# Optimization experiments

Measured on AMD Instinct MI355X. Metric: run time of the kernel, lower is better.

Reference implementation:

```python
import jax, jax.numpy as jnp
import numpy as np
import math

N, L, D, H = 8192, 64, 256, 4
DH = D // H
TAU = 300.0

def setup_inputs() -> dict:
    key = jax.random.key(0)
    ks = jax.random.split(key, 16)
    tokens = jax.random.normal(ks[0], (N, L, D), dtype=jnp.float32)
    # sorted random timestamps in seconds within each patch window
    ts = jnp.sort(jax.random.uniform(ks[1], (N, L, 1), dtype=jnp.float32) * 3600.0, axis=1)
    mask = (jax.random.uniform(ks[2], (N, L, 1), dtype=jnp.float32) < 0.9).astype(jnp.float32)
    mask = mask.at[:, 0, :].set(1.0)  # guarantee at least one valid key per row
    s = 0.02
    Wq = jax.random.normal(ks[3], (D, D), dtype=jnp.float32) * s
    bq = jnp.zeros((D,), dtype=jnp.float32)
    Wk = jax.random.normal(ks[4], (D, D), dtype=jnp.float32) * s
    bk = jnp.zeros((D,), dtype=jnp.float32)
    Wv = jax.random.normal(ks[5], (D, D), dtype=jnp.float32) * s
    bv = jnp.zeros((D,), dtype=jnp.float32)
    Wo = jax.random.normal(ks[6], (D, D), dtype=jnp.float32) * s
    bo = jnp.zeros((D,), dtype=jnp.float32)
    readout = jax.random.normal(ks[7], (D,), dtype=jnp.float32)
    return {"tokens": tokens, "ts": ts, "mask": mask,
            "Wq": Wq, "bq": bq, "Wk": Wk, "bk": bk, "Wv": Wv, "bv": bv,
            "Wo": Wo, "bo": bo, "readout": readout}

def reference(tokens, ts, mask, Wq, bq, Wk, bk, Wv, bv, Wo, bo, readout):
    n, l, d = tokens.shape
    scale = 1.0 / math.sqrt(DH)
    # time-decay bias: dt = |t_i - t_j|, bias = log(exp(-dt/tau) + 1e-12)
    t = ts[..., 0]                                   # (N, L)
    dt = jnp.abs(t[:, :, None] - t[:, None, :])      # (N, L, L)
    bias = jnp.log(jnp.exp(-dt / max(TAU, 1e-6)) + 1e-12)
    def proj(x, W, b):
        return (x @ W.T + b).reshape(n, l, H, DH).transpose(0, 2, 1, 3)  # (N,H,L,DH)
    q = proj(tokens, Wq, bq)
    k = proj(tokens, Wk, bk)
    v = proj(tokens, Wv, bv)
    attn = jnp.einsum('nhqd,nhkd->nhqk', q, k) * scale + bias[:, None, :, :]
    key_pad = mask[..., 0] <= 0                      # (N, L) True = pad
    attn = jnp.where(key_pad[:, None, None, :], -1e9, attn)
    A = jax.nn.softmax(attn, axis=-1)
    out = jnp.einsum('nhqk,nhkd->nhqd', A, v).transpose(0, 2, 1, 3).reshape(n, l, d)
    out = (out @ Wo.T + bo) * mask                   # (N, L, D)
    # learned-query pooling attention over timesteps
    qh = jnp.broadcast_to(readout.reshape(1, 1, d), (n, 1, d)).reshape(n, 1, H, DH).transpose(0, 2, 1, 3)
    kh = out.reshape(n, l, H, DH).transpose(0, 2, 1, 3)  # kh == vh
    pool = jnp.einsum('nhqd,nhkd->nhqk', qh, kh) * scale  # (N,H,1,L)
    pool = jnp.where(key_pad[:, None, None, :], -1e9, pool)
    P = jax.nn.softmax(pool, axis=-1)
    pooled = jnp.einsum('nhqk,nhkd->nhqd', P, kh).transpose(0, 2, 1, 3).reshape(n, d)
    return pooled
```

## Files before the change

kernel.cpp:

```cpp
#include <hip/hip_runtime.h>
#include <hip/hip_bf16.h>


typedef __attribute__((ext_vector_type(8))) short short8;
typedef __attribute__((ext_vector_type(4))) float f32x4;

__device__ __forceinline__ unsigned short f2b(float x) {
  unsigned int u = __float_as_uint(x);
  u += 0x7FFFu + ((u >> 16) & 1u);
  return (unsigned short)(u >> 16);
}
__device__ __forceinline__ float b2f(unsigned short b) {
  return __uint_as_float(((unsigned int)b) << 16);
}

__global__ void wconv_kernel(const float* __restrict__ Wq, const float* __restrict__ Wk,
                             const float* __restrict__ Wv, const float* __restrict__ Wo,
                             unsigned short* __restrict__ dst) {
  int e = blockIdx.x * 256 + threadIdx.x;
  int row = e >> 8, col = e & 255;
  float v;
  if (row < 256)      v = Wq[(row << 8) | col];
  else if (row < 512) v = Wk[((row - 256) << 8) | col];
  else if (row < 768) v = Wv[((row - 512) << 8) | col];
  else                v = Wo[((row - 768) << 8) | col];
  dst[e] = f2b(v);
}

__global__ __launch_bounds__(256, 2) void patch_attn_kernel(
    const float* __restrict__ tokens, const float* __restrict__ ts,
    const float* __restrict__ maskp,
    const unsigned short* __restrict__ Wqkv,
    const unsigned short* __restrict__ Wob,
    const float* __restrict__ bq, const float* __restrict__ bk,
    const float* __restrict__ bv, const float* __restrict__ bo,
    const float* __restrict__ readout, float* __restrict__ outp) {
  __shared__ unsigned short Xb[64][264];
  __shared__ unsigned short Qh[64][72];
  __shared__ unsigned short Kh[64][72];
  __shared__ unsigned short VhT[64][72];
  __shared__ unsigned short Ah[64][72];
  __shared__ float tl[64];
  __shared__ float ml[64];
  __shared__ float ps[4][64];

  const int n   = blockIdx.x;
  const int tid = threadIdx.x;
  const int w   = tid >> 6;
  const int l   = tid & 63;
  const int l16 = l & 15;
  const int lq  = l >> 4;

  if (tid < 64) { tl[tid] = ts[n * 64 + tid]; ml[tid] = maskp[n * 64 + tid]; }

  const float4* Xg = (const float4*)(tokens + (size_t)n * (64 * 256));
  #pragma unroll
  for (int it = 0; it < 16; ++it) {
    int p = tid + it * 256;
    float4 v = Xg[p];
    int row = p >> 6, col = (p & 63) << 2;
    ushort4 b;
    b.x = f2b(v.x); b.y = f2b(v.y); b.z = f2b(v.z); b.w = f2b(v.w);
    *(ushort4*)&Xb[row][col] = b;
  }
  __syncthreads();

  const f32x4 fz = {0.f, 0.f, 0.f, 0.f};
  f32x4 oacc[4][4];
  #pragma unroll
  for (int a = 0; a < 4; ++a)
    #pragma unroll
    for (int bb = 0; bb < 4; ++bb) oacc[a][bb] = fz;

  #pragma unroll 1
  for (int h = 0; h < 4; ++h) {
    f32x4 qacc[4][3];
    #pragma unroll
    for (int rf = 0; rf < 4; ++rf)
      #pragma unroll
      for (int c = 0; c < 3; ++c) qacc[rf][c] = fz;

    const unsigned short* wp0 = Wqkv + (size_t)((0 * 256 + h * 64 + 16 * w + l16) * 256 + lq * 8);
    const unsigned short* wp1 = Wqkv + (size_t)((1 * 256 + h * 64 + 16 * w + l16) * 256 + lq * 8);
    const unsigned short* wp2 = Wqkv + (size_t)((2 * 256 + h * 64 + 16 * w + l16) * 256 + lq * 8);

    #pragma unroll
    for (int ks = 0; ks < 8; ++ks) {
      int k0 = ks * 32;
      short8 afr[4];
      #pragma unroll
      for (int rf = 0; rf < 4; ++rf)
        afr[rf] = *(const short8*)&Xb[16 * rf + l16][k0 + lq * 8];
      short8 bfr[3];
      bfr[0] = *(const short8*)(wp0 + k0);
      bfr[1] = *(const short8*)(wp1 + k0);
      bfr[2] = *(const short8*)(wp2 + k0);
      #pragma unroll
      for (int rf = 0; rf < 4; ++rf) {
        qacc[rf][0] = __builtin_amdgcn_mfma_f32_16x16x32_bf16(afr[rf], bfr[0], qacc[rf][0], 0, 0, 0);
        qacc[rf][1] = __builtin_amdgcn_mfma_f32_16x16x32_bf16(afr[rf], bfr[1], qacc[rf][1], 0, 0, 0);
        qacc[rf][2] = __builtin_amdgcn_mfma_f32_16x16x32_bf16(afr[rf], bfr[2], qacc[rf][2], 0, 0, 0);
      }
    }
    {
      int ncol = 16 * w + l16;
      float bqv = bq[h * 64 + ncol], bkv = bk[h * 64 + ncol], bvv = bv[h * 64 + ncol];
      #pragma unroll
      for (int rf = 0; rf < 4; ++rf) {
        #pragma unroll
        for (int i = 0; i < 4; ++i) {
          int m = 16 * rf + lq * 4 + i;
          Qh[m][ncol]  = f2b(qacc[rf][0][i] + bqv);
          Kh[m][ncol]  = f2b(qacc[rf][1][i] + bkv);
          VhT[ncol][m] = f2b(qacc[rf][2][i] + bvv);
        }
      }
    }
    __syncthreads();

    f32x4 sacc[4];
    #pragma unroll
    for (int j = 0; j < 4; ++j) sacc[j] = fz;
    #pragma unroll
    for (int ks = 0; ks < 2; ++ks) {
      int k0 = ks * 32;
      short8 aq = *(const short8*)&Qh[16 * w + l16][k0 + lq * 8];
      #pragma unroll
      for (int j = 0; j < 4; ++j) {
        short8 bk8 = *(const short8*)&Kh[16 * j + l16][k0 + lq * 8];
        sacc[j] = __builtin_amdgcn_mfma_f32_16x16x32_bf16(aq, bk8, sacc[j], 0, 0, 0);
      }
    }
    {
      float tn[4], mn[4];
      #pragma unroll
      for (int j = 0; j < 4; ++j) { tn[j] = tl[16 * j + l16]; mn[j] = ml[16 * j + l16]; }
      #pragma unroll
      for (int i = 0; i < 4; ++i) {
        int m = 16 * w + lq * 4 + i;
        float tm = tl[m];
        float sv[4];
        #pragma unroll
        for (int j = 0; j < 4; ++j) {
          float s = sacc[j][i] * 0.125f - fabsf(tm - tn[j]) * (1.0f / 300.0f);
          sv[j] = (mn[j] <= 0.0f) ? -1e9f : s;
        }
        float mx = fmaxf(fmaxf(sv[0], sv[1]), fmaxf(sv[2], sv[3]));
        #pragma unroll
        for (int x = 1; x < 16; x <<= 1) mx = fmaxf(mx, __shfl_xor(mx, x));
        float pj[4], sum = 0.f;
        #pragma unroll
        for (int j = 0; j < 4; ++j) { pj[j] = __expf(sv[j] - mx); sum += pj[j]; }
        #pragma unroll
        for (int x = 1; x < 16; x <<= 1) sum += __shfl_xor(sum, x);
        float inv = 1.0f / sum;
        #pragma unroll
        for (int j = 0; j < 4; ++j) Ah[m][16 * j + l16] = f2b(pj[j] * inv);
      }
    }
    __syncthreads();

    f32x4 pacc[4];
    #pragma unroll
    for (int j = 0; j < 4; ++j) pacc[j] = fz;
    #pragma unroll
    for (int ks = 0; ks < 2; ++ks) {
      int k0 = ks * 32;
      short8 ap = *(const short8*)&Ah[16 * w + l16][k0 + lq * 8];
      #pragma unroll
      for (int j = 0; j < 4; ++j) {
        short8 bv8 = *(const short8*)&VhT[16 * j + l16][k0 + lq * 8];
        pacc[j] = __builtin_amdgcn_mfma_f32_16x16x32_bf16(ap, bv8, pacc[j], 0, 0, 0);
      }
    }
    #pragma unroll
    for (int j = 0; j < 4; ++j)
      #pragma unroll
      for (int i = 0; i < 4; ++i)
        Qh[16 * w + lq * 4 + i][16 * j + l16] = f2b(pacc[j][i]);
    __syncthreads();

    {
      const unsigned short* wop[4];
      #pragma unroll
      for (int j = 0; j < 4; ++j)
        wop[j] = Wob + (size_t)((64 * w + 16 * j + l16) * 256 + h * 64 + lq * 8);
      #pragma unroll
      for (int ks = 0; ks < 2; ++ks) {
        int k0 = ks * 32;
        short8 ao[4];
        #pragma unroll
        for (int rf = 0; rf < 4; ++rf)
          ao[rf] = *(const short8*)&Qh[16 * rf + l16][k0 + lq * 8];
        short8 bw[4];
        #pragma unroll
        for (int j = 0; j < 4; ++j) bw[j] = *(const short8*)(wop[j] + k0);
        #pragma unroll
        for (int rf = 0; rf < 4; ++rf)
          #pragma unroll
          for (int j = 0; j < 4; ++j)
            oacc[rf][j] = __builtin_amdgcn_mfma_f32_16x16x32_bf16(ao[rf], bw[j], oacc[rf][j], 0, 0, 0);
      }
    }
    __syncthreads();
  }

  #pragma unroll
  for (int rf = 0; rf < 4; ++rf) {
    #pragma unroll
    for (int j = 0; j < 4; ++j) {
      int ncol = 64 * w + 16 * j + l16;
      float bov = bo[ncol];
      #pragma unroll
      for (int i = 0; i < 4; ++i) {
        int m = 16 * rf + lq * 4 + i;
        Xb[m][ncol] = f2b((oacc[rf][j][i] + bov) * ml[m]);
      }
    }
  }
  __syncthreads();

  {
    float acc = 0.f;
    #pragma unroll
    for (int d0 = 0; d0 < 64; d0 += 4) {
      ushort4 o4 = *(const ushort4*)&Xb[l][w * 64 + d0];
      acc += b2f(o4.x) * readout[w * 64 + d0]
           + b2f(o4.y) * readout[w * 64 + d0 + 1]
           + b2f(o4.z) * readout[w * 64 + d0 + 2]
           + b2f(o4.w) * readout[w * 64 + d0 + 3];
    }
    float logit = acc * 0.125f;
    if (ml[l] <= 0.0f) logit = -1e9f;
    float mx = logit;
    #pragma unroll
    for (int x = 1; x < 64; x <<= 1) mx = fmaxf(mx, __shfl_xor(mx, x));
    float p = __expf(logit - mx);
    float sm = p;
    #pragma unroll
    for (int x = 1; x < 64; x <<= 1) sm += __shfl_xor(sm, x);
    ps[w][l] = p / sm;
  }
  __syncthreads();
  {
    float o = 0.f;
    #pragma unroll
    for (int k = 0; k < 64; ++k) o += ps[w][k] * b2f(Xb[k][w * 64 + l]);
    outp[(size_t)n * 256 + w * 64 + l] = o;
  }
}

extern "C" void kernel_launch(void* const* d_in, const int* in_sizes, int n_in,
                              void* d_out, int out_size, void* d_ws, size_t ws_size,
                              hipStream_t stream) {
  const float* tokens  = (const float*)d_in[0];
  const float* ts      = (const float*)d_in[1];
  const float* mask    = (const float*)d_in[2];
  const float* Wq      = (const float*)d_in[3];
  const float* bq      = (const float*)d_in[4];
  const float* Wk      = (const float*)d_in[5];
  const float* bk      = (const float*)d_in[6];
  const float* Wv      = (const float*)d_in[7];
  const float* bv      = (const float*)d_in[8];
  const float* Wo      = (const float*)d_in[9];
  const float* bo      = (const float*)d_in[10];
  const float* readout = (const float*)d_in[11];
  (void)n_in; (void)out_size; (void)ws_size;

  unsigned short* Wqkv_b = (unsigned short*)d_ws;
  unsigned short* Wo_b   = Wqkv_b + 768 * 256;

  const int n_patches = in_sizes[0] / (64 * 256);

  wconv_kernel<<<1024, 256, 0, stream>>>(Wq, Wk, Wv, Wo, Wqkv_b);
  patch_attn_kernel<<<n_patches, 256, 0, stream>>>(
      tokens, ts, mask, Wqkv_b, Wo_b, bq, bk, bv, bo, readout, (float*)d_out);
}
```

Before: 1.293 ms.

## Stream tokens from global into MFMA fragments and shrink LDS for higher occupancy

```diff
diff --git a/kernel.cpp b/kernel.cpp
--- a/kernel.cpp
+++ b/kernel.cpp
@@ -12,6 +12,14 @@
 }
 __device__ __forceinline__ float b2f(unsigned short b) {
   return __uint_as_float(((unsigned int)b) << 16);
+}
+__device__ __forceinline__ short8 pack8(float4 a, float4 b) {
+  short8 r;
+  r[0] = (short)f2b(a.x); r[1] = (short)f2b(a.y);
+  r[2] = (short)f2b(a.z); r[3] = (short)f2b(a.w);
+  r[4] = (short)f2b(b.x); r[5] = (short)f2b(b.y);
+  r[6] = (short)f2b(b.z); r[7] = (short)f2b(b.w);
+  return r;
 }
 
 __global__ void wconv_kernel(const float* __restrict__ Wq, const float* __restrict__ Wk,
@@ -27,7 +35,7 @@
   dst[e] = f2b(v);
 }
 
-__global__ __launch_bounds__(256, 2) void patch_attn_kernel(
+__global__ __launch_bounds__(256, 3) void patch_attn_kernel(
     const float* __restrict__ tokens, const float* __restrict__ ts,
     const float* __restrict__ maskp,
     const unsigned short* __restrict__ Wqkv,
@@ -35,13 +43,8 @@
     const float* __restrict__ bq, const float* __restrict__ bk,
     const float* __restrict__ bv, const float* __restrict__ bo,
     const float* __restrict__ readout, float* __restrict__ outp) {
-  __shared__ unsigned short Xb[64][264];
-  __shared__ unsigned short Qh[64][72];
-  __shared__ unsigned short Kh[64][72];
-  __shared__ unsigned short VhT[64][72];
-  __shared__ unsigned short Ah[64][72];
-  __shared__ float tl[64];
-  __shared__ float ml[64];
+  __shared__ unsigned short T[4][64][72];
+  __shared__ float tl[64], ml[64], mneg[64];
   __shared__ float ps[4][64];
 
   const int n   = blockIdx.x;
@@ -51,133 +54,144 @@
   const int l16 = l & 15;
   const int lq  = l >> 4;
 
-  if (tid < 64) { tl[tid] = ts[n * 64 + tid]; ml[tid] = maskp[n * 64 + tid]; }
-
-  const float4* Xg = (const float4*)(tokens + (size_t)n * (64 * 256));
-  #pragma unroll
-  for (int it = 0; it < 16; ++it) {
-    int p = tid + it * 256;
-    float4 v = Xg[p];
-    int row = p >> 6, col = (p & 63) << 2;
-    ushort4 b;
-    b.x = f2b(v.x); b.y = f2b(v.y); b.z = f2b(v.z); b.w = f2b(v.w);
-    *(ushort4*)&Xb[row][col] = b;
+  if (tid < 64) {
+    tl[tid] = ts[n * 64 + tid];
+    float mk = maskp[n * 64 + tid];
+    ml[tid]   = mk;
+    mneg[tid] = (mk > 0.0f) ? 0.0f : -1e9f;
   }
   __syncthreads();
+
+  const float4* Xg4 = (const float4*)(tokens + (size_t)n * (64 * 256));
+  const float tq = tl[16 * w + l16];
 
   const f32x4 fz = {0.f, 0.f, 0.f, 0.f};
   f32x4 oacc[4][4];
   #pragma unroll
   for (int a = 0; a < 4; ++a)
     #pragma unroll
-    for (int bb = 0; bb < 4; ++bb) oacc[a][bb] = fz;
+    for (int b = 0; b < 4; ++b) oacc[a][b] = fz;
 
   #pragma unroll 1
   for (int h = 0; h < 4; ++h) {
-    f32x4 qacc[4][3];
-    #pragma unroll
-    for (int rf = 0; rf < 4; ++rf)
-      #pragma unroll
-      for (int c = 0; c < 3; ++c) qacc[rf][c] = fz;
-
-    const unsigned short* wp0 = Wqkv + (size_t)((0 * 256 + h * 64 + 16 * w + l16) * 256 + lq * 8);
-    const unsigned short* wp1 = Wqkv + (size_t)((1 * 256 + h * 64 + 16 * w + l16) * 256 + lq * 8);
-    const unsigned short* wp2 = Wqkv + (size_t)((2 * 256 + h * 64 + 16 * w + l16) * 256 + lq * 8);
+    f32x4 qac[4], kac[4], vac[4];
+    #pragma unroll
+    for (int j = 0; j < 4; ++j) { qac[j] = fz; kac[j] = fz; vac[j] = fz; }
+
+    const unsigned short* wqp = Wqkv + (size_t)((0 * 256 + h * 64 + 16 * w + l16) * 256 + lq * 8);
+    const unsigned short* wkp = Wqkv + (size_t)((1 * 256 + h * 64 + 16 * w + l16) * 256 + lq * 8);
+    const unsigned short* wvp = Wqkv + (size_t)((2 * 256 + h * 64 + 16 * w + l16) * 256 + lq * 8);
 
     #pragma unroll
     for (int ks = 0; ks < 8; ++ks) {
-      int k0 = ks * 32;
-      short8 afr[4];
+      short8 xf[4];
+      #pragma unroll
+      for (int rf = 0; rf < 4; ++rf) {
+        const float4* p = Xg4 + (16 * rf + l16) * 64 + ks * 8 + lq * 2;
+        xf[rf] = pack8(p[0], p[1]);
+      }
+      short8 wq = *(const short8*)(wqp + ks * 32);
+      short8 wk = *(const short8*)(wkp + ks * 32);
+      short8 wv = *(const short8*)(wvp + ks * 32);
+      #pragma unroll
+      for (int j = 0; j < 4; ++j)
+        qac[j] = __builtin_amdgcn_mfma_f32_16x16x32_bf16(wq, xf[j], qac[j], 0, 0, 0);
+      #pragma unroll
+      for (int j = 0; j < 4; ++j)
+        kac[j] = __builtin_amdgcn_mfma_f32_16x16x32_bf16(wk, xf[j], kac[j], 0, 0, 0);
       #pragma unroll
       for (int rf = 0; rf < 4; ++rf)
-        afr[rf] = *(const short8*)&Xb[16 * rf + l16][k0 + lq * 8];
-      short8 bfr[3];
-      bfr[0] = *(const short8*)(wp0 + k0);
-      bfr[1] = *(const short8*)(wp1 + k0);
-      bfr[2] = *(const short8*)(wp2 + k0);
+        vac[rf] = __builtin_amdgcn_mfma_f32_16x16x32_bf16(xf[rf], wv, vac[rf], 0, 0, 0);
+    }
+    {
+      float4 bq4 = *(const float4*)&bq[h * 64 + 16 * w + 4 * lq];
+      float4 bk4 = *(const float4*)&bk[h * 64 + 16 * w + 4 * lq];
+      float  bvv = bv[h * 64 + 16 * w + l16];
+      #pragma unroll
+      for (int j = 0; j < 4; ++j) {
+        ushort4 q4, k4;
+        q4.x = f2b(qac[j][0] + bq4.x); q4.y = f2b(qac[j][1] + bq4.y);
+        q4.z = f2b(qac[j][2] + bq4.z); q4.w = f2b(qac[j][3] + bq4.w);
+        *(ushort4*)&T[0][16 * j + l16][16 * w + 4 * lq] = q4;
+        k4.x = f2b(kac[j][0] + bk4.x); k4.y = f2b(kac[j][1] + bk4.y);
+        k4.z = f2b(kac[j][2] + bk4.z); k4.w = f2b(kac[j][3] + bk4.w);
+        *(ushort4*)&T[1][16 * j + l16][16 * w + 4 * lq] = k4;
+      }
       #pragma unroll
       for (int rf = 0; rf < 4; ++rf) {
-        qacc[rf][0] = __builtin_amdgcn_mfma_f32_16x16x32_bf16(afr[rf], bfr[0], qacc[rf][0], 0, 0, 0);
-        qacc[rf][1] = __builtin_amdgcn_mfma_f32_16x16x32_bf16(afr[rf], bfr[1], qacc[rf][1], 0, 0, 0);
-        qacc[rf][2] = __builtin_amdgcn_mfma_f32_16x16x32_bf16(afr[rf], bfr[2], qacc[rf][2], 0, 0, 0);
+        ushort4 v4;
+        v4.x = f2b(vac[rf][0] + bvv); v4.y = f2b(vac[rf][1] + bvv);
+        v4.z = f2b(vac[rf][2] + bvv); v4.w = f2b(vac[rf][3] + bvv);
+        *(ushort4*)&T[2][16 * w + l16][16 * rf + 4 * lq] = v4;
+      }
+    }
+    __syncthreads();
+
+    f32x4 sac[4];
+    #pragma unroll
+    for (int j = 0; j < 4; ++j) sac[j] = fz;
+    #pragma unroll
+    for (int ks = 0; ks < 2; ++ks) {
+      short8 qf = *(const short8*)&T[0][16 * w + l16][ks * 32 + lq * 8];
+      #pragma unroll
+      for (int j = 0; j < 4; ++j) {
+        short8 kf = *(const short8*)&T[1][16 * j + l16][ks * 32 + lq * 8];
+        sac[j] = __builtin_amdgcn_mfma_f32_16x16x32_bf16(kf, qf, sac[j], 0, 0, 0);
       }
     }
     {
-      int ncol = 16 * w + l16;
-      float bqv = bq[h * 64 + ncol], bkv = bk[h * 64 + ncol], bvv = bv[h * 64 + ncol];
-      #pragma unroll
-      for (int rf = 0; rf < 4; ++rf) {
-        #pragma unroll
-        for (int i = 0; i < 4; ++i) {
-          int m = 16 * rf + lq * 4 + i;
-          Qh[m][ncol]  = f2b(qacc[rf][0][i] + bqv);
-          Kh[m][ncol]  = f2b(qacc[rf][1][i] + bkv);
-          VhT[ncol][m] = f2b(qacc[rf][2][i] + bvv);
-        }
-      }
-    }
-    __syncthreads();
-
-    f32x4 sacc[4];
-    #pragma unroll
-    for (int j = 0; j < 4; ++j) sacc[j] = fz;
+      float sv[4][4], mx = -3e38f;
+      #pragma unroll
+      for (int j = 0; j < 4; ++j) {
+        float4 t4 = *(const float4*)&tl[16 * j + 4 * lq];
+        float4 m4 = *(const float4*)&mneg[16 * j + 4 * lq];
+        float s0 = sac[j][0] * 0.125f - fabsf(tq - t4.x) * (1.0f / 300.0f) + m4.x;
+        float s1 = sac[j][1] * 0.125f - fabsf(tq - t4.y) * (1.0f / 300.0f) + m4.y;
+        float s2 = sac[j][2] * 0.125f - fabsf(tq - t4.z) * (1.0f / 300.0f) + m4.z;
+        float s3 = sac[j][3] * 0.125f - fabsf(tq - t4.w) * (1.0f / 300.0f) + m4.w;
+        sv[j][0] = s0; sv[j][1] = s1; sv[j][2] = s2; sv[j][3] = s3;
+        mx = fmaxf(mx, fmaxf(fmaxf(s0, s1), fmaxf(s2, s3)));
+      }
+      mx = fmaxf(mx, __shfl_xor(mx, 16));
+      mx = fmaxf(mx, __shfl_xor(mx, 32));
+      float pv[4][4], sum = 0.f;
+      #pragma unroll
+      for (int j = 0; j < 4; ++j)
+        #pragma unroll
+        for (int i = 0; i < 4; ++i) { float e = __expf(sv[j][i] - mx); pv[j][i] = e; sum += e; }
+      sum += __shfl_xor(sum, 16);
+      sum += __shfl_xor(sum, 32);
+      float inv = 1.0f / sum;
+      #pragma unroll
+      for (int j = 0; j < 4; ++j) {
+        ushort4 a4;
+        a4.x = f2b(pv[j][0] * inv); a4.y = f2b(pv[j][1] * inv);
+        a4.z = f2b(pv[j][2] * inv); a4.w = f2b(pv[j][3] * inv);
+        *(ushort4*)&T[3][16 * w + l16][16 * j + 4 * lq] = a4;
+      }
+    }
+    __syncthreads();
+
+    f32x4 oc[4];
+    #pragma unroll
+    for (int j = 0; j < 4; ++j) oc[j] = fz;
     #pragma unroll
     for (int ks = 0; ks < 2; ++ks) {
-      int k0 = ks * 32;
-      short8 aq = *(const short8*)&Qh[16 * w + l16][k0 + lq * 8];
-      #pragma unroll
-      for (int j = 0; j < 4; ++j) {
-        short8 bk8 = *(const short8*)&Kh[16 * j + l16][k0 + lq * 8];
-        sacc[j] = __builtin_amdgcn_mfma_f32_16x16x32_bf16(aq, bk8, sacc[j], 0, 0, 0);
-      }
-    }
-    {
-      float tn[4], mn[4];
-      #pragma unroll
-      for (int j = 0; j < 4; ++j) { tn[j] = tl[16 * j + l16]; mn[j] = ml[16 * j + l16]; }
-      #pragma unroll
-      for (int i = 0; i < 4; ++i) {
-        int m = 16 * w + lq * 4 + i;
-        float tm = tl[m];
-        float sv[4];
-        #pragma unroll
-        for (int j = 0; j < 4; ++j) {
-          float s = sacc[j][i] * 0.125f - fabsf(tm - tn[j]) * (1.0f / 300.0f);
-          sv[j] = (mn[j] <= 0.0f) ? -1e9f : s;
-        }
-        float mx = fmaxf(fmaxf(sv[0], sv[1]), fmaxf(sv[2], sv[3]));
-        #pragma unroll
-        for (int x = 1; x < 16; x <<= 1) mx = fmaxf(mx, __shfl_xor(mx, x));
-        float pj[4], sum = 0.f;
-        #pragma unroll
-        for (int j = 0; j < 4; ++j) { pj[j] = __expf(sv[j] - mx); sum += pj[j]; }
-        #pragma unroll
-        for (int x = 1; x < 16; x <<= 1) sum += __shfl_xor(sum, x);
-        float inv = 1.0f / sum;
-        #pragma unroll
-        for (int j = 0; j < 4; ++j) Ah[m][16 * j + l16] = f2b(pj[j] * inv);
-      }
-    }
-    __syncthreads();
-
-    f32x4 pacc[4];
-    #pragma unroll
-    for (int j = 0; j < 4; ++j) pacc[j] = fz;
-    #pragma unroll
-    for (int ks = 0; ks < 2; ++ks) {
-      int k0 = ks * 32;
-      short8 ap = *(const short8*)&Ah[16 * w + l16][k0 + lq * 8];
-      #pragma unroll
-      for (int j = 0; j < 4; ++j) {
-        short8 bv8 = *(const short8*)&VhT[16 * j + l16][k0 + lq * 8];
-        pacc[j] = __builtin_amdgcn_mfma_f32_16x16x32_bf16(ap, bv8, pacc[j], 0, 0, 0);
-      }
-    }
-    #pragma unroll
-    for (int j = 0; j < 4; ++j)
-      #pragma unroll
-      for (int i = 0; i < 4; ++i)
-        Qh[16 * w + lq * 4 + i][16 * j + l16] = f2b(pacc[j][i]);
+      short8 vf = *(const short8*)&T[2][16 * w + l16][ks * 32 + lq * 8];
+      #pragma unroll
+      for (int j = 0; j < 4; ++j) {
+        short8 af = *(const short8*)&T[3][16 * j + l16][ks * 32 + lq * 8];
+        oc[j] = __builtin_amdgcn_mfma_f32_16x16x32_bf16(vf, af, oc[j], 0, 0, 0);
+      }
+    }
+    __syncthreads();
+    #pragma unroll
+    for (int j = 0; j < 4; ++j) {
+      ushort4 o4;
+      o4.x = f2b(oc[j][0]); o4.y = f2b(oc[j][1]);
+      o4.z = f2b(oc[j][2]); o4.w = f2b(oc[j][3]);
+      *(ushort4*)&T[0][16 * j + l16][16 * w + 4 * lq] = o4;
+    }
     __syncthreads();
 
     {
@@ -187,14 +201,13 @@
         wop[j] = Wob + (size_t)((64 * w + 16 * j + l16) * 256 + h * 64 + lq * 8);
       #pragma unroll
       for (int ks = 0; ks < 2; ++ks) {
-        int k0 = ks * 32;
         short8 ao[4];
         #pragma unroll
         for (int rf = 0; rf < 4; ++rf)
-          ao[rf] = *(const short8*)&Qh[16 * rf + l16][k0 + lq * 8];
+          ao[rf] = *(const short8*)&T[0][16 * rf + l16][ks * 32 + lq * 8];
         short8 bw[4];
         #pragma unroll
-        for (int j = 0; j < 4; ++j) bw[j] = *(const short8*)(wop[j] + k0);
+        for (int j = 0; j < 4; ++j) bw[j] = *(const short8*)(wop[j] + ks * 32);
         #pragma unroll
         for (int rf = 0; rf < 4; ++rf)
           #pragma unroll
@@ -206,16 +219,17 @@
   }
 
   #pragma unroll
-  for (int rf = 0; rf < 4; ++rf) {
-    #pragma unroll
-    for (int j = 0; j < 4; ++j) {
-      int ncol = 64 * w + 16 * j + l16;
-      float bov = bo[ncol];
-      #pragma unroll
-      for (int i = 0; i < 4; ++i) {
-        int m = 16 * rf + lq * 4 + i;
-        Xb[m][ncol] = f2b((oacc[rf][j][i] + bov) * ml[m]);
-      }
+  for (int j = 0; j < 4; ++j) {
+    float bov = bo[64 * w + 16 * j + l16];
+    #pragma unroll
+    for (int rf = 0; rf < 4; ++rf) {
+      float4 m4 = *(const float4*)&ml[16 * rf + 4 * lq];
+      ushort4 t4;
+      t4.x = f2b((oacc[rf][j][0] + bov) * m4.x);
+      t4.y = f2b((oacc[rf][j][1] + bov) * m4.y);
+      t4.z = f2b((oacc[rf][j][2] + bov) * m4.z);
+      t4.w = f2b((oacc[rf][j][3] + bov) * m4.w);
+      *(ushort4*)&T[w][16 * j + l16][16 * rf + 4 * lq] = t4;
     }
   }
   __syncthreads();
@@ -223,15 +237,9 @@
   {
     float acc = 0.f;
     #pragma unroll
-    for (int d0 = 0; d0 < 64; d0 += 4) {
-      ushort4 o4 = *(const ushort4*)&Xb[l][w * 64 + d0];
-      acc += b2f(o4.x) * readout[w * 64 + d0]
-           + b2f(o4.y) * readout[w * 64 + d0 + 1]
-           + b2f(o4.z) * readout[w * 64 + d0 + 2]
-           + b2f(o4.w) * readout[w * 64 + d0 + 3];
-    }
-    float logit = acc * 0.125f;
-    if (ml[l] <= 0.0f) logit = -1e9f;
+    for (int d = 0; d < 64; ++d)
+      acc += b2f(T[w][d][l]) * readout[64 * w + d];
+    float logit = acc * 0.125f + mneg[l];
     float mx = logit;
     #pragma unroll
     for (int x = 1; x < 64; x <<= 1) mx = fmaxf(mx, __shfl_xor(mx, x));
@@ -245,8 +253,12 @@
   {
     float o = 0.f;
     #pragma unroll
-    for (int k = 0; k < 64; ++k) o += ps[w][k] * b2f(Xb[k][w * 64 + l]);
-    outp[(size_t)n * 256 + w * 64 + l] = o;
+    for (int kc = 0; kc < 16; ++kc) {
+      ushort4 t4 = *(const ushort4*)&T[w][l][kc * 4];
+      o += ps[w][kc * 4 + 0] * b2f(t4.x) + ps[w][kc * 4 + 1] * b2f(t4.y)
+         + ps[w][kc * 4 + 2] * b2f(t4.z) + ps[w][kc * 4 + 3] * b2f(t4.w);
+    }
+    outp[(size_t)n * 256 + 64 * w + l] = o;
   }
 }
 
```

Result: slower. 1.946 ms (+50.5%).
